# Optimization experiments

Measured on AMD Instinct MI355X. Metric: run time of the kernel, lower is better.

Reference implementation:

```python
import jax, jax.numpy as jnp
import numpy as np

N = 200000      # nodes
E_EDGES = 600000
G = 8000        # graphs
F_IN = 16
EMB = 128
L = 5           # GIN layers
C = 12          # targets
BN_EPS = 1e-5


def _bn(x, s, b, m, v):
    # BatchNorm1d in eval mode: normalize with stored running stats
    return (x - m) * jax.lax.rsqrt(v + BN_EPS) * s + b


def _mlp(x, w1, b1, s1, bb1, m1, v1, w2, b2, s2, bb2, m2, v2):
    h = jax.nn.relu(_bn(x @ w1 + b1, s1, bb1, m1, v1))
    return jax.nn.relu(_bn(h @ w2 + b2, s2, bb2, m2, v2))


def setup_inputs() -> dict:
    key = jax.random.key(0)
    ks = iter(jax.random.split(key, 64))
    inp = {}
    def nrm(shape, fan):
        return (jax.random.normal(next(ks), shape, jnp.float32) / np.sqrt(fan)).astype(jnp.float32)
    def bn_set(name, shape):
        inp[name + '_scale'] = jax.random.uniform(next(ks), shape, jnp.float32) * 0.5 + 0.75
        inp[name + '_bias'] = jax.random.normal(next(ks), shape, jnp.float32) * 0.1
        inp[name + '_mean'] = jax.random.normal(next(ks), shape, jnp.float32) * 0.1
        inp[name + '_var'] = jax.random.uniform(next(ks), shape, jnp.float32) * 0.5 + 0.75

    inp['x'] = jax.random.normal(next(ks), (N, F_IN), jnp.float32)
    src = jax.random.randint(next(ks), (E_EDGES,), 0, N, jnp.int32)
    dst = jax.random.randint(next(ks), (E_EDGES,), 0, N, jnp.int32)
    inp['edge_index'] = jnp.stack([src, dst])
    # sorted batch ids; every graph gets at least one node (avoid empty segment_max)
    inp['batch'] = jnp.sort(jnp.concatenate([
        jnp.arange(G, dtype=jnp.int32),
        jax.random.randint(next(ks), (N - G,), 0, G, jnp.int32)]))

    inp['init_w1'] = nrm((F_IN, EMB), F_IN)
    inp['init_b1'] = jnp.zeros((EMB,), jnp.float32)
    bn_set('init_bn1', (EMB,))
    inp['init_w2'] = nrm((EMB, EMB), EMB)
    inp['init_b2'] = jnp.zeros((EMB,), jnp.float32)
    bn_set('init_bn2', (EMB,))
    inp['init_lin_w'] = nrm((EMB, C), EMB)
    inp['init_lin_b'] = jnp.zeros((C,), jnp.float32)
    inp['eps'] = jnp.zeros((L,), jnp.float32)  # train_eps init 0.0
    inp['lw1'] = nrm((L, EMB, EMB), EMB)
    inp['lb1'] = jnp.zeros((L, EMB), jnp.float32)
    bn_set('lbn1', (L, EMB))
    inp['lw2'] = nrm((L, EMB, EMB), EMB)
    inp['lb2'] = jnp.zeros((L, EMB), jnp.float32)
    bn_set('lbn2', (L, EMB))
    inp['llin_w'] = nrm((L, EMB, C), EMB)
    inp['llin_b'] = jnp.zeros((L, C), jnp.float32)
    return inp


def _forward(edge_index, batch, x, init_w1, init_b1, init_bn1_scale, init_bn1_bias,
             init_bn1_mean, init_bn1_var, init_w2, init_b2, init_bn2_scale,
             init_bn2_bias, init_bn2_mean, init_bn2_var, init_lin_w, init_lin_b,
             eps, lw1, lb1, lbn1_scale, lbn1_bias, lbn1_mean, lbn1_var,
             lw2, lb2, lbn2_scale, lbn2_bias, lbn2_mean, lbn2_var, llin_w, llin_b):
    src, dst = edge_index[0], edge_index[1]
    h = _mlp(x, init_w1, init_b1, init_bn1_scale, init_bn1_bias, init_bn1_mean,
             init_bn1_var, init_w2, init_b2, init_bn2_scale, init_bn2_bias,
             init_bn2_mean, init_bn2_var)  # [N, EMB]
    # initial readout: linear then global max pool over graphs
    out = jax.ops.segment_max(h @ init_lin_w + init_lin_b, batch, num_segments=G)  # [G, C]
    for l in range(L):
        # GINConv: h <- MLP((1+eps)*h + sum_{j in N(i)} h_j)
        agg = jax.ops.segment_sum(h[src], dst, num_segments=N)  # gather + scatter-add
        h = _mlp((1.0 + eps[l]) * h + agg,
                 lw1[l], lb1[l], lbn1_scale[l], lbn1_bias[l], lbn1_mean[l], lbn1_var[l],
                 lw2[l], lb2[l], lbn2_scale[l], lbn2_bias[l], lbn2_mean[l], lbn2_var[l])
        # per-layer readout: global max pool then linear
        out = out + jax.ops.segment_max(h, batch, num_segments=G) @ llin_w[l] + llin_b[l]
    return out


def reference(x, edge_index, batch, init_w1, init_b1, init_bn1_scale, init_bn1_bias,
              init_bn1_mean, init_bn1_var, init_w2, init_b2, init_bn2_scale,
              init_bn2_bias, init_bn2_mean, init_bn2_var, init_lin_w, init_lin_b,
              eps, lw1, lb1, lbn1_scale, lbn1_bias, lbn1_mean, lbn1_var,
              lw2, lb2, lbn2_scale, lbn2_bias, lbn2_mean, lbn2_var, llin_w, llin_b):
    return _forward(edge_index, batch, x, init_w1, init_b1, init_bn1_scale,
                    init_bn1_bias, init_bn1_mean, init_bn1_var, init_w2, init_b2,
                    init_bn2_scale, init_bn2_bias, init_bn2_mean, init_bn2_var,
                    init_lin_w, init_lin_b, eps, lw1, lb1, lbn1_scale, lbn1_bias,
                    lbn1_mean, lbn1_var, lw2, lb2, lbn2_scale, lbn2_bias,
                    lbn2_mean, lbn2_var, llin_w, llin_b)
```

## Files before the change

kernel.cpp:

```cpp
#include <hip/hip_runtime.h>
#include <hip/hip_bf16.h>
#include <math.h>

#define EMB 128
#define CDIM 12
#define FIN 16
#define NLAYER 5
#define BN_EPS 1e-5f

typedef __attribute__((ext_vector_type(8))) _Float16 f16x8;
typedef __attribute__((ext_vector_type(2))) __fp16 fp16v2;
typedef __attribute__((ext_vector_type(4))) float f32x4;
typedef unsigned short ushort_t;

union h2u { fp16v2 h; unsigned u; };
union hu  { _Float16 h; ushort_t u; };

__device__ __forceinline__ void fsplit2(float a, float b, unsigned& hi, unsigned& lo) {
    h2u H; H.h = __builtin_amdgcn_cvt_pkrtz(a, b);
    float r0 = a - (float)H.h.x;
    float r1 = b - (float)H.h.y;
    h2u L; L.h = __builtin_amdgcn_cvt_pkrtz(r0, r1);
    hi = H.u; lo = L.u;
}

__device__ __forceinline__ unsigned pkrn(float x, float y) {
    hu A; A.h = (_Float16)x;
    hu B; B.h = (_Float16)y;
    return (unsigned)A.u | ((unsigned)B.u << 16);
}

__device__ __forceinline__ void acc8(float* f, uint4 v) {
    h2u c0, c1, c2, c3;
    c0.u = v.x; c1.u = v.y; c2.u = v.z; c3.u = v.w;
    f[0] += (float)c0.h.x; f[1] += (float)c0.h.y;
    f[2] += (float)c1.h.x; f[3] += (float)c1.h.y;
    f[4] += (float)c2.h.x; f[5] += (float)c2.h.y;
    f[6] += (float)c3.h.x; f[7] += (float)c3.h.y;
}

__device__ __forceinline__ unsigned swz(int node, unsigned byteoff) {
    return (unsigned)(node * 256 + byteoff) ^ (((unsigned)node & 7u) << 4);
}


__global__ __launch_bounds__(256) void k_gstart(const int* __restrict__ batch,
                                                int* __restrict__ gs, int N, int G) {
    int i = blockIdx.x * 256 + threadIdx.x;
    if (i >= N) return;
    if (i == 0) gs[0] = 0;
    else { int b = batch[i]; if (b != batch[i - 1]) gs[b] = i; }
    if (i == N - 1) gs[G] = N;
}

__global__ __launch_bounds__(256) void k_zero_i32(int* __restrict__ p, int n) {
    int i = blockIdx.x * 256 + threadIdx.x;
    if (i < n) p[i] = 0;
}

__global__ __launch_bounds__(256) void k_fill_i32(int* __restrict__ p, int val, int n) {
    int i = blockIdx.x * 256 + threadIdx.x;
    if (i < n) p[i] = val;
}

__global__ __launch_bounds__(256) void k_zero_f32(float* __restrict__ p, int n) {
    int i = blockIdx.x * 256 + threadIdx.x;
    if (i < n) p[i] = 0.f;
}

__global__ __launch_bounds__(128) void k_zero_dummy(ushort_t* __restrict__ a,
                                                    ushort_t* __restrict__ b, int N) {
    int i = threadIdx.x;
    a[(size_t)N * EMB + i] = 0;
    b[(size_t)N * EMB + i] = 0;
}

__global__ __launch_bounds__(256) void k_hist(const int* __restrict__ dst, int* __restrict__ cnt, int E) {
    int e = blockIdx.x * 256 + threadIdx.x;
    if (e < E) atomicAdd(&cnt[dst[e]], 1);
}

__global__ __launch_bounds__(256) void k_scan1(const int* __restrict__ cnt, int* __restrict__ rs,
                                               int* __restrict__ partials, int N) {
    __shared__ int tsum[256];
    int t = threadIdx.x;
    int base = blockIdx.x * 1024 + t * 4;
    int c[4];
    #pragma unroll
    for (int j = 0; j < 4; j++) c[j] = (base + j < N) ? ((cnt[base + j] + 3) & ~3) : 0;
    int s = c[0] + c[1] + c[2] + c[3];
    tsum[t] = s;
    __syncthreads();
    for (int off = 1; off < 256; off <<= 1) {
        int v = (t >= off) ? tsum[t - off] : 0;
        __syncthreads();
        tsum[t] += v;
        __syncthreads();
    }
    int run = tsum[t] - s;
    if (t == 255) partials[blockIdx.x] = tsum[255];
    #pragma unroll
    for (int j = 0; j < 4; j++) {
        if (base + j <= N) rs[base + j] = run;
        run += c[j];
    }
}

__global__ __launch_bounds__(256) void k_scan2(int* __restrict__ partials, int NB) {
    __shared__ int tmp[256];
    int t = threadIdx.x;
    int v = (t < NB) ? partials[t] : 0;
    tmp[t] = v;
    __syncthreads();
    for (int off = 1; off < 256; off <<= 1) {
        int u = (t >= off) ? tmp[t - off] : 0;
        __syncthreads();
        tmp[t] += u;
        __syncthreads();
    }
    if (t < NB) partials[t] = tmp[t] - v;
}

__global__ __launch_bounds__(256) void k_scan3(int* __restrict__ rs, const int* __restrict__ partials,
                                               int* __restrict__ cur_off, int N) {
    int t = threadIdx.x;
    int base = blockIdx.x * 1024 + t * 4;
    int add = partials[blockIdx.x];
    #pragma unroll
    for (int j = 0; j < 4; j++) {
        int i = base + j;
        if (i <= N) {
            int v = rs[i] + add;
            rs[i] = v;
            if (i < N) cur_off[i] = v;
        }
    }
}

__global__ __launch_bounds__(256) void k_fillslots(const int* __restrict__ src, const int* __restrict__ dst,
                                                   int* __restrict__ cur_off, int* __restrict__ csr_src, int E) {
    int e = blockIdx.x * 256 + threadIdx.x;
    if (e >= E) return;
    int d = dst[e];
    int pos = atomicAdd(&cur_off[d], 1);
    csr_src[pos] = src[e];
}


__global__ __launch_bounds__(256) void k_prep(
        const float* __restrict__ init_w1, const float* __restrict__ init_b1,
        const float* __restrict__ b1s, const float* __restrict__ b1b,
        const float* __restrict__ b1m, const float* __restrict__ b1v,
        const float* __restrict__ init_w2, const float* __restrict__ init_b2,
        const float* __restrict__ i_s, const float* __restrict__ i_b,
        const float* __restrict__ i_m, const float* __restrict__ i_v,
        const float* __restrict__ lw1, const float* __restrict__ lb1,
        const float* __restrict__ l1s, const float* __restrict__ l1b,
        const float* __restrict__ l1m, const float* __restrict__ l1v,
        const float* __restrict__ lw2, const float* __restrict__ lb2,
        const float* __restrict__ l2s, const float* __restrict__ l2b,
        const float* __restrict__ l2m, const float* __restrict__ l2v,
        const float* __restrict__ ilin_w, const float* __restrict__ ilin_b,
        ushort_t* __restrict__ WT, float* __restrict__ biasf,
        float* __restrict__ W1f, float* __restrict__ bias1f,
        ushort_t* __restrict__ WzT, float* __restrict__ biasz) {
    int j = blockIdx.x;
    int t = threadIdx.x;
    __shared__ float alpha[EMB];

    if (j == 12) {
        if (t < 16) biasz[t] = (t < CDIM) ? ilin_b[t] : 0.f;
        for (int i = t; i < 16 * EMB; i += 256) {
            int f = i >> 7, k = i & 127;
            float w = (f < CDIM) ? ilin_w[k * CDIM + f] : 0.f;
            hu x; x.h = (_Float16)w;
            WzT[i] = x.u;
        }
        return;
    }
    if (j == 11) {
        if (t < EMB) {
            float a = b1s[t] * rsqrtf(b1v[t] + BN_EPS);
            alpha[t] = a;
            bias1f[t] = init_b1[t] * a + (b1b[t] - b1m[t] * a);
        }
        __syncthreads();
        for (int i = t; i < FIN * EMB; i += 256) W1f[i] = init_w1[i] * alpha[i & 127];
        return;
    }

    const float *W, *lb, *s, *bb, *m, *v;
    if (j == 0)      { W = init_w2;            lb = init_b2;        s = i_s;           bb = i_b;           m = i_m;           v = i_v; }
    else if (j <= 5) { int l = j - 1; W = lw1 + l * 16384; lb = lb1 + l * 128; s = l1s + l * 128; bb = l1b + l * 128; m = l1m + l * 128; v = l1v + l * 128; }
    else             { int l = j - 6; W = lw2 + l * 16384; lb = lb2 + l * 128; s = l2s + l * 128; bb = l2b + l * 128; m = l2m + l * 128; v = l2v + l * 128; }
    if (t < EMB) {
        float a = s[t] * rsqrtf(v[t] + BN_EPS);
        alpha[t] = a;
        biasf[j * EMB + t] = lb[t] * a + (bb[t] - m[t] * a);
    }
    __syncthreads();
    for (int i = t; i < EMB * EMB; i += 256) {
        int k = i >> 7, f = i & 127;
        float w = W[i] * alpha[f];
        hu x; x.h = (_Float16)w;
        WT[j * 16384 + f * 128 + k] = x.u;
    }
}


template<int MODE>
__global__ __launch_bounds__(512, 4) void k_layer(
        const float* __restrict__ xin, const ushort_t* __restrict__ hin,
        ushort_t* __restrict__ hout, float* __restrict__ z,
        const ushort_t* __restrict__ W1T, const float* __restrict__ b1,
        const ushort_t* __restrict__ W2T, const float* __restrict__ b2,
        const ushort_t* __restrict__ WzT, const float* __restrict__ bz,
        const float* __restrict__ W1f, const float* __restrict__ b1f,
        const int* __restrict__ rs, const int* __restrict__ csr, const float* __restrict__ epsp,
        const int* __restrict__ batch, float* __restrict__ smax,
        int ntiles, int N) {
    constexpr int NT = (MODE == 1) ? 32 : 16;
    __shared__ ushort_t Ah[NT * 128], Al[NT * 128], Bh_[NT * 128], Bl_[NT * 128];
    __shared__ float W1s[(MODE == 0) ? FIN * EMB : 1];

    const int t = threadIdx.x;
    const int w = t >> 6;
    const int lane = t & 63;
    const int col = lane & 15, kg = lane >> 4;

    if (MODE == 0) {
        for (int i = t; i < FIN * EMB; i += 512) W1s[i] = W1f[i];
        __syncthreads();
    }

    f16x8 w1f[4], w2f[4], wzf[4];
    #pragma unroll
    for (int s = 0; s < 4; s++) {
        int off = (w * 16 + col) * EMB + s * 32 + kg * 8;
        w1f[s] = *(const f16x8*)(W1T + off);
        if (MODE == 1) w2f[s] = *(const f16x8*)(W2T + off);
        if (MODE == 0) {
            int zoff = col * EMB + s * 32 + kg * 8;
            wzf[s] = *(const f16x8*)(WzT + zoff);
        }
    }
    float4 bv1 = *(const float4*)&b1[w * 16 + kg * 4];
    float4 bv2, bvz;
    if (MODE == 1) bv2 = *(const float4*)&b2[w * 16 + kg * 4];
    if (MODE == 0) bvz = *(const float4*)&bz[kg * 4];
    float se = (MODE == 1) ? (1.f + epsp[0]) : 0.f;

    for (int tile = blockIdx.x; tile < ntiles; tile += gridDim.x) {
        const int n0 = tile * NT;

        if (MODE == 1) {
            const int nl = t >> 4, q2 = t & 15;
            const int nc = min(n0 + nl, N - 1);
            const uint4* hp = (const uint4*)hin;
            uint4 sv = hp[(size_t)nc * 16 + q2];
            float a[8] = {0.f, 0.f, 0.f, 0.f, 0.f, 0.f, 0.f, 0.f};
            acc8(a, sv);
            #pragma unroll
            for (int i = 0; i < 8; i++) a[i] *= se;
            int p = rs[nc], pe = rs[nc + 1];
            for (; p < pe; p += 4) {
                uint4 idx = *(const uint4*)&csr[p];
                uint4 v0 = hp[(size_t)idx.x * 16 + q2];
                uint4 v1 = hp[(size_t)idx.y * 16 + q2];
                uint4 v2 = hp[(size_t)idx.z * 16 + q2];
                uint4 v3 = hp[(size_t)idx.w * 16 + q2];
                acc8(a, v0); acc8(a, v1); acc8(a, v2); acc8(a, v3);
            }
            uint4 H, L;
            fsplit2(a[0], a[1], H.x, L.x);
            fsplit2(a[2], a[3], H.y, L.y);
            fsplit2(a[4], a[5], H.z, L.z);
            fsplit2(a[6], a[7], H.w, L.w);
            unsigned ad = swz(nl, (unsigned)q2 * 16);
            *(uint4*)((char*)Ah + ad) = H;
            *(uint4*)((char*)Al + ad) = L;
        } else {
            const int nl = t >> 5, q = t & 31;
            const int nc = min(n0 + nl, N - 1);
            float4 ba = *(const float4*)&b1f[q * 4];
            float a0 = ba.x, a1 = ba.y, a2 = ba.z, a3 = ba.w;
            const float* xp = xin + (size_t)nc * FIN;
            #pragma unroll
            for (int k = 0; k < FIN; k++) {
                float xk = xp[k];
                float4 wv = *(const float4*)&W1s[k * EMB + q * 4];
                a0 += xk * wv.x; a1 += xk * wv.y; a2 += xk * wv.z; a3 += xk * wv.w;
            }
            a0 = fmaxf(a0, 0.f); a1 = fmaxf(a1, 0.f); a2 = fmaxf(a2, 0.f); a3 = fmaxf(a3, 0.f);
            uint2 H, L;
            fsplit2(a0, a1, H.x, L.x);
            fsplit2(a2, a3, H.y, L.y);
            unsigned ad = swz(nl, (unsigned)q * 8);
            *(uint2*)((char*)Ah + ad) = H;
            *(uint2*)((char*)Al + ad) = L;
        }
        __syncthreads();

        {
            f32x4 aA0 = (f32x4){0.f, 0.f, 0.f, 0.f}, aB0 = aA0, aA1 = aA0, aB1 = aA0;
            #pragma unroll
            for (int s = 0; s < 4; s++) {
                unsigned bo = (unsigned)((s * 32 + kg * 8) * 2);
                f16x8 xh0 = *(const f16x8*)((const char*)Ah + swz(col, bo));
                f16x8 xl0 = *(const f16x8*)((const char*)Al + swz(col, bo));
                aA0 = __builtin_amdgcn_mfma_f32_16x16x32_f16(w1f[s], xh0, aA0, 0, 0, 0);
                aB0 = __builtin_amdgcn_mfma_f32_16x16x32_f16(w1f[s], xl0, aB0, 0, 0, 0);
                if (MODE == 1) {
                    f16x8 xh1 = *(const f16x8*)((const char*)Ah + swz(col + 16, bo));
                    f16x8 xl1 = *(const f16x8*)((const char*)Al + swz(col + 16, bo));
                    aA1 = __builtin_amdgcn_mfma_f32_16x16x32_f16(w1f[s], xh1, aA1, 0, 0, 0);
                    aB1 = __builtin_amdgcn_mfma_f32_16x16x32_f16(w1f[s], xl1, aB1, 0, 0, 0);
                }
            }
            #pragma unroll
            for (int sub = 0; sub < ((MODE == 1) ? 2 : 1); sub++) {
                f32x4 aa = sub ? aA1 : aA0, ab = sub ? aB1 : aB0;
                float y0 = fmaxf(aa[0] + ab[0] + bv1.x, 0.f);
                float y1 = fmaxf(aa[1] + ab[1] + bv1.y, 0.f);
                float y2 = fmaxf(aa[2] + ab[2] + bv1.z, 0.f);
                float y3 = fmaxf(aa[3] + ab[3] + bv1.w, 0.f);
                if (MODE == 0) {
                    int onode = n0 + col;
                    if (onode < N) {
                        uint2 P; P.x = pkrn(y0, y1); P.y = pkrn(y2, y3);
                        *(uint2*)&hout[(size_t)onode * EMB + w * 16 + kg * 4] = P;
                    }
                }
                uint2 H, L;
                fsplit2(y0, y1, H.x, L.x);
                fsplit2(y2, y3, H.y, L.y);
                unsigned ad = swz(col + sub * 16, (unsigned)(w * 32 + kg * 8));
                *(uint2*)((char*)Bh_ + ad) = H;
                *(uint2*)((char*)Bl_ + ad) = L;
            }
        }
        __syncthreads();

        if (MODE == 1) {
            f32x4 aA0 = (f32x4){0.f, 0.f, 0.f, 0.f}, aB0 = aA0, aA1 = aA0, aB1 = aA0;
            #pragma unroll
            for (int s = 0; s < 4; s++) {
                unsigned bo = (unsigned)((s * 32 + kg * 8) * 2);
                f16x8 xh0 = *(const f16x8*)((const char*)Bh_ + swz(col, bo));
                f16x8 xl0 = *(const f16x8*)((const char*)Bl_ + swz(col, bo));
                f16x8 xh1 = *(const f16x8*)((const char*)Bh_ + swz(col + 16, bo));
                f16x8 xl1 = *(const f16x8*)((const char*)Bl_ + swz(col + 16, bo));
                aA0 = __builtin_amdgcn_mfma_f32_16x16x32_f16(w2f[s], xh0, aA0, 0, 0, 0);
                aB0 = __builtin_amdgcn_mfma_f32_16x16x32_f16(w2f[s], xl0, aB0, 0, 0, 0);
                aA1 = __builtin_amdgcn_mfma_f32_16x16x32_f16(w2f[s], xh1, aA1, 0, 0, 0);
                aB1 = __builtin_amdgcn_mfma_f32_16x16x32_f16(w2f[s], xl1, aB1, 0, 0, 0);
            }
            #pragma unroll
            for (int sub = 0; sub < 2; sub++) {
                f32x4 aa = sub ? aA1 : aA0, ab = sub ? aB1 : aB0;
                int onode = n0 + col + sub * 16;
                float o0 = fmaxf(aa[0] + ab[0] + bv2.x, 0.f);
                float o1 = fmaxf(aa[1] + ab[1] + bv2.y, 0.f);
                float o2 = fmaxf(aa[2] + ab[2] + bv2.z, 0.f);
                float o3 = fmaxf(aa[3] + ab[3] + bv2.w, 0.f);
                if (hout && onode < N) {
                    uint2 P; P.x = pkrn(o0, o1); P.y = pkrn(o2, o3);
                    *(uint2*)&hout[(size_t)onode * EMB + w * 16 + kg * 4] = P;
                }
                bool valid = onode < N;
                float v0 = valid ? o0 : 0.f, v1 = valid ? o1 : 0.f;
                float v2 = valid ? o2 : 0.f, v3 = valid ? o3 : 0.f;
                int g = batch[min(onode, N - 1)];
                #pragma unroll
                for (int off = 1; off < 16; off <<= 1) {
                    float u0 = __shfl_up(v0, off, 16);
                    float u1 = __shfl_up(v1, off, 16);
                    float u2 = __shfl_up(v2, off, 16);
                    float u3 = __shfl_up(v3, off, 16);
                    int gg = __shfl_up(g, off, 16);
                    bool take = (col >= off) && (gg == g);
                    if (take) {
                        v0 = fmaxf(v0, u0); v1 = fmaxf(v1, u1);
                        v2 = fmaxf(v2, u2); v3 = fmaxf(v3, u3);
                    }
                }
                int gn = __shfl_down(g, 1, 16);
                bool tail = (col == 15) || (gn != g);
                if (tail) {
                    unsigned* sp = (unsigned*)&smax[(size_t)g * EMB + w * 16 + kg * 4];
                    atomicMax(sp + 0, __float_as_uint(v0));
                    atomicMax(sp + 1, __float_as_uint(v1));
                    atomicMax(sp + 2, __float_as_uint(v2));
                    atomicMax(sp + 3, __float_as_uint(v3));
                }
            }
        } else if (w == 0) {
            f32x4 aA0 = (f32x4){0.f, 0.f, 0.f, 0.f}, aB0 = aA0;
            #pragma unroll
            for (int s = 0; s < 4; s++) {
                unsigned bo = (unsigned)((s * 32 + kg * 8) * 2);
                f16x8 xh = *(const f16x8*)((const char*)Bh_ + swz(col, bo));
                f16x8 xl = *(const f16x8*)((const char*)Bl_ + swz(col, bo));
                aA0 = __builtin_amdgcn_mfma_f32_16x16x32_f16(wzf[s], xh, aA0, 0, 0, 0);
                aB0 = __builtin_amdgcn_mfma_f32_16x16x32_f16(wzf[s], xl, aB0, 0, 0, 0);
            }
            int onode = n0 + col;
            if (onode < N && kg < 3) {
                float4 o;
                o.x = aA0[0] + aB0[0] + bvz.x;
                o.y = aA0[1] + aB0[1] + bvz.y;
                o.z = aA0[2] + aB0[2] + bvz.z;
                o.w = aA0[3] + aB0[3] + bvz.w;
                *(float4*)&z[(size_t)onode * CDIM + kg * 4] = o;
            }
        }
    }
}


__global__ __launch_bounds__(64) void k_zmax(const float* __restrict__ z, const int* __restrict__ gs,
        float* __restrict__ out, int G) {
    int g = blockIdx.x;
    int t = threadIdx.x;
    if (t >= CDIM) return;
    int s0 = gs[g], e0 = gs[g + 1];
    float m = -INFINITY;
    for (int n = s0; n < e0; n++) m = fmaxf(m, z[(size_t)n * CDIM + t]);
    out[g * CDIM + t] = m;
}

__global__ __launch_bounds__(128) void k_comb(const float* __restrict__ smax,
        const float* __restrict__ llin_w, const float* __restrict__ llin_b,
        float* __restrict__ out, int G) {
    int g = blockIdx.x;
    int t = threadIdx.x;
    __shared__ float mv[NLAYER][EMB];
    #pragma unroll
    for (int l = 0; l < NLAYER; l++)
        mv[l][t] = smax[((size_t)l * G + g) * EMB + t];
    __syncthreads();
    __shared__ float parts_[8][16];
    int c = t & 15, half = t >> 4;
    float acc = 0.f;
    if (c < CDIM) {
        #pragma unroll
        for (int l = 0; l < NLAYER; l++) {
            const float* Wl = llin_w + l * EMB * CDIM;
            #pragma unroll
            for (int kk = 0; kk < 16; kk++) {
                int k = half * 16 + kk;
                acc += mv[l][k] * Wl[k * CDIM + c];
            }
        }
    }
    parts_[half][c] = acc;
    __syncthreads();
    if (t < CDIM) {
        float s = 0.f;
        #pragma unroll
        for (int hh = 0; hh < 8; hh++) s += parts_[hh][t];
        #pragma unroll
        for (int l = 0; l < NLAYER; l++) s += llin_b[l * CDIM + t];
        out[g * CDIM + t] += s;
    }
}


extern "C" void kernel_launch(void* const* d_in, const int* in_sizes, int n_in,
                              void* d_out, int out_size, void* d_ws, size_t ws_size,
                              hipStream_t stream) {
    const float* x        = (const float*)d_in[0];
    const int*   ei       = (const int*)d_in[1];
    const int*   batch    = (const int*)d_in[2];
    const float* init_w1  = (const float*)d_in[3];
    const float* init_b1  = (const float*)d_in[4];
    const float* ibn1_s   = (const float*)d_in[5];
    const float* ibn1_b   = (const float*)d_in[6];
    const float* ibn1_m   = (const float*)d_in[7];
    const float* ibn1_v   = (const float*)d_in[8];
    const float* init_w2  = (const float*)d_in[9];
    const float* init_b2  = (const float*)d_in[10];
    const float* ibn2_s   = (const float*)d_in[11];
    const float* ibn2_b   = (const float*)d_in[12];
    const float* ibn2_m   = (const float*)d_in[13];
    const float* ibn2_v   = (const float*)d_in[14];
    const float* ilin_w   = (const float*)d_in[15];
    const float* ilin_b   = (const float*)d_in[16];
    const float* eps      = (const float*)d_in[17];
    const float* lw1      = (const float*)d_in[18];
    const float* lb1      = (const float*)d_in[19];
    const float* lbn1_s   = (const float*)d_in[20];
    const float* lbn1_b   = (const float*)d_in[21];
    const float* lbn1_m   = (const float*)d_in[22];
    const float* lbn1_v   = (const float*)d_in[23];
    const float* lw2      = (const float*)d_in[24];
    const float* lb2      = (const float*)d_in[25];
    const float* lbn2_s   = (const float*)d_in[26];
    const float* lbn2_b   = (const float*)d_in[27];
    const float* lbn2_m   = (const float*)d_in[28];
    const float* lbn2_v   = (const float*)d_in[29];
    const float* llin_w   = (const float*)d_in[30];
    const float* llin_b   = (const float*)d_in[31];

    const int N = in_sizes[0] / FIN;
    const int E = in_sizes[1] / 2;
    const int G = out_size / CDIM;
    const int* src = ei;
    const int* dst = ei + E;
    float* out = (float*)d_out;

    const int EPADMAX = E + 3 * N;

    char* wp = (char*)d_ws;
    auto alloc = [&](size_t bytes) { char* p = wp; wp += (bytes + 255) & ~(size_t)255; return p; };
    ushort_t* WT    = (ushort_t*)alloc((size_t)11 * 16384 * 2);
    float*    biasf = (float*)alloc(11 * EMB * 4);
    float*    W1f   = (float*)alloc(FIN * EMB * 4);
    float*    bias1f= (float*)alloc(EMB * 4);
    ushort_t* WzT   = (ushort_t*)alloc(16 * EMB * 2);
    float*    biasz = (float*)alloc(16 * 4);
    int*      gs    = (int*)alloc((size_t)(G + 1) * 4);
    int*      rs    = (int*)alloc((size_t)(N + 1) * 4);
    int*      curoff= (int*)alloc((size_t)N * 4);
    int*      csr   = (int*)alloc((size_t)EPADMAX * 4);
    int*      parts = (int*)alloc(256 * 4);
    float*    zbuf  = (float*)alloc((size_t)N * CDIM * 4);
    float*    smax  = (float*)alloc((size_t)NLAYER * G * EMB * 4);
    ushort_t* bufP  = (ushort_t*)alloc((size_t)(N + 1) * EMB * 2);
    ushort_t* bufQ  = (ushort_t*)alloc((size_t)(N + 1) * EMB * 2);
    int*      cnt   = csr;

    const int NB = (N + 1 + 1023) / 1024;
    const int ntiles16 = (N + 15) / 16;
    const int ntiles32 = (N + 31) / 32;
    const int GRID = 2084;

    k_zero_f32<<<((NLAYER * G * EMB) + 255) / 256, 256, 0, stream>>>(smax, NLAYER * G * EMB);
    k_zero_dummy<<<1, 128, 0, stream>>>(bufP, bufQ, N);

    k_zero_i32<<<(N + 255) / 256, 256, 0, stream>>>(cnt, N);
    k_hist<<<(E + 255) / 256, 256, 0, stream>>>(dst, cnt, E);
    k_scan1<<<NB, 256, 0, stream>>>(cnt, rs, parts, N);
    k_scan2<<<1, 256, 0, stream>>>(parts, NB);
    k_scan3<<<NB, 256, 0, stream>>>(rs, parts, curoff, N);
    k_fill_i32<<<(EPADMAX + 255) / 256, 256, 0, stream>>>(csr, N, EPADMAX);
    k_fillslots<<<(E + 255) / 256, 256, 0, stream>>>(src, dst, curoff, csr, E);
    k_gstart<<<(N + 255) / 256, 256, 0, stream>>>(batch, gs, N, G);
    k_prep<<<13, 256, 0, stream>>>(init_w1, init_b1, ibn1_s, ibn1_b, ibn1_m, ibn1_v,
                                   init_w2, init_b2, ibn2_s, ibn2_b, ibn2_m, ibn2_v,
                                   lw1, lb1, lbn1_s, lbn1_b, lbn1_m, lbn1_v,
                                   lw2, lb2, lbn2_s, lbn2_b, lbn2_m, lbn2_v,
                                   ilin_w, ilin_b,
                                   WT, biasf, W1f, bias1f, WzT, biasz);

    k_layer<0><<<GRID, 512, 0, stream>>>(x, nullptr, bufQ, zbuf,
                                         WT, biasf,
                                         nullptr, nullptr,
                                         WzT, biasz,
                                         W1f, bias1f,
                                         nullptr, nullptr, nullptr,
                                         nullptr, nullptr, ntiles16, N);
    k_zmax<<<G, 64, 0, stream>>>(zbuf, gs, out, G);

    ushort_t* cur = bufQ;
    ushort_t* oth = bufP;
    for (int l = 0; l < NLAYER; l++) {
        ushort_t* houtl = (l == NLAYER - 1) ? nullptr : oth;
        k_layer<1><<<GRID, 512, 0, stream>>>(nullptr, cur, houtl, nullptr,
                                             WT + (size_t)(1 + l) * 16384, biasf + (1 + l) * EMB,
                                             WT + (size_t)(6 + l) * 16384, biasf + (6 + l) * EMB,
                                             nullptr, nullptr,
                                             nullptr, nullptr,
                                             rs, csr, eps + l,
                                             batch, smax + (size_t)l * G * EMB, ntiles32, N);
        ushort_t* tmp = cur; cur = oth; oth = tmp;
    }
    k_comb<<<G, 128, 0, stream>>>(smax, llin_w, llin_b, out, G);
}
```

Measured before the change: 711.9 us.

## Enlarge GIN layer tile to 64 nodes and issue neighbor gathers early

Raises the node tile in the message-passing layer kernel from 32 to 64, so each thread aggregates two nodes. The first group of four neighbor rows for both nodes is loaded before any accumulation, giving more gathers in flight per thread. The MFMA stages loop over four 16-node subtiles that share the register-held weights, and the grid becomes about two tiles per block. This doubles LDS use per block and adds register pressure under the 512x4 launch bounds, which may reduce occupancy.

```diff
diff --git a/kernel.cpp b/kernel.cpp
--- a/kernel.cpp
+++ b/kernel.cpp
@@ -219,7 +219,8 @@
         const int* __restrict__ rs, const int* __restrict__ csr, const float* __restrict__ epsp,
         const int* __restrict__ batch, float* __restrict__ smax,
         int ntiles, int N) {
-    constexpr int NT = (MODE == 1) ? 32 : 16;
+    constexpr int NT = (MODE == 1) ? 64 : 16;
+    constexpr int NSUB = (MODE == 1) ? 4 : 1;
     __shared__ ushort_t Ah[NT * 128], Al[NT * 128], Bh_[NT * 128], Bl_[NT * 128];
     __shared__ float W1s[(MODE == 0) ? FIN * EMB : 1];
 
@@ -250,33 +251,55 @@
     if (MODE == 0) bvz = *(const float4*)&bz[kg * 4];
     float se = (MODE == 1) ? (1.f + epsp[0]) : 0.f;
 
+    const int nlp = t >> 4, q2p = t & 15;
+
     for (int tile = blockIdx.x; tile < ntiles; tile += gridDim.x) {
         const int n0 = tile * NT;
 
         if (MODE == 1) {
-            const int nl = t >> 4, q2 = t & 15;
-            const int nc = min(n0 + nl, N - 1);
             const uint4* hp = (const uint4*)hin;
-            uint4 sv = hp[(size_t)nc * 16 + q2];
-            float a[8] = {0.f, 0.f, 0.f, 0.f, 0.f, 0.f, 0.f, 0.f};
-            acc8(a, sv);
-            #pragma unroll
-            for (int i = 0; i < 8; i++) a[i] *= se;
-            int p = rs[nc], pe = rs[nc + 1];
-            for (; p < pe; p += 4) {
+            const int ncA = min(n0 + nlp, N - 1);
+            const int ncB = min(n0 + nlp + 32, N - 1);
+            uint4 svA = hp[(size_t)ncA * 16 + q2p];
+            uint4 svB = hp[(size_t)ncB * 16 + q2p];
+            int pA = rs[ncA], peA = rs[ncA + 1];
+            int pB = rs[ncB], peB = rs[ncB + 1];
+            uint4 iA, iB;
+            if (pA < peA) iA = *(const uint4*)&csr[pA];
+            else { iA.x = iA.y = iA.z = iA.w = (unsigned)N; }
+            if (pB < peB) iB = *(const uint4*)&csr[pB];
+            else { iB.x = iB.y = iB.z = iB.w = (unsigned)N; }
+            uint4 rA0 = hp[(size_t)iA.x * 16 + q2p], rA1 = hp[(size_t)iA.y * 16 + q2p];
+            uint4 rA2 = hp[(size_t)iA.z * 16 + q2p], rA3 = hp[(size_t)iA.w * 16 + q2p];
+            uint4 rB0 = hp[(size_t)iB.x * 16 + q2p], rB1 = hp[(size_t)iB.y * 16 + q2p];
+            uint4 rB2 = hp[(size_t)iB.z * 16 + q2p], rB3 = hp[(size_t)iB.w * 16 + q2p];
+
+            float a[8] = {0.f,0.f,0.f,0.f,0.f,0.f,0.f,0.f};
+            float b[8] = {0.f,0.f,0.f,0.f,0.f,0.f,0.f,0.f};
+            acc8(a, svA); acc8(b, svB);
+            #pragma unroll
+            for (int i = 0; i < 8; i++) { a[i] *= se; b[i] *= se; }
+            acc8(a, rA0); acc8(a, rA1); acc8(a, rA2); acc8(a, rA3);
+            acc8(b, rB0); acc8(b, rB1); acc8(b, rB2); acc8(b, rB3);
+            for (int p = pA + 4; p < peA; p += 4) {
                 uint4 idx = *(const uint4*)&csr[p];
-                uint4 v0 = hp[(size_t)idx.x * 16 + q2];
-                uint4 v1 = hp[(size_t)idx.y * 16 + q2];
-                uint4 v2 = hp[(size_t)idx.z * 16 + q2];
-                uint4 v3 = hp[(size_t)idx.w * 16 + q2];
-                acc8(a, v0); acc8(a, v1); acc8(a, v2); acc8(a, v3);
+                acc8(a, hp[(size_t)idx.x * 16 + q2p]); acc8(a, hp[(size_t)idx.y * 16 + q2p]);
+                acc8(a, hp[(size_t)idx.z * 16 + q2p]); acc8(a, hp[(size_t)idx.w * 16 + q2p]);
+            }
+            for (int p = pB + 4; p < peB; p += 4) {
+                uint4 idx = *(const uint4*)&csr[p];
+                acc8(b, hp[(size_t)idx.x * 16 + q2p]); acc8(b, hp[(size_t)idx.y * 16 + q2p]);
+                acc8(b, hp[(size_t)idx.z * 16 + q2p]); acc8(b, hp[(size_t)idx.w * 16 + q2p]);
             }
             uint4 H, L;
-            fsplit2(a[0], a[1], H.x, L.x);
-            fsplit2(a[2], a[3], H.y, L.y);
-            fsplit2(a[4], a[5], H.z, L.z);
-            fsplit2(a[6], a[7], H.w, L.w);
-            unsigned ad = swz(nl, (unsigned)q2 * 16);
+            fsplit2(a[0], a[1], H.x, L.x); fsplit2(a[2], a[3], H.y, L.y);
+            fsplit2(a[4], a[5], H.z, L.z); fsplit2(a[6], a[7], H.w, L.w);
+            unsigned ad = swz(nlp, (unsigned)q2p * 16);
+            *(uint4*)((char*)Ah + ad) = H;
+            *(uint4*)((char*)Al + ad) = L;
+            fsplit2(b[0], b[1], H.x, L.x); fsplit2(b[2], b[3], H.y, L.y);
+            fsplit2(b[4], b[5], H.z, L.z); fsplit2(b[6], b[7], H.w, L.w);
+            ad = swz(nlp + 32, (unsigned)q2p * 16);
             *(uint4*)((char*)Ah + ad) = H;
             *(uint4*)((char*)Al + ad) = L;
         } else {
@@ -302,28 +325,26 @@
         __syncthreads();
 
         {
-            f32x4 aA0 = (f32x4){0.f, 0.f, 0.f, 0.f}, aB0 = aA0, aA1 = aA0, aB1 = aA0;
+            f32x4 aA[NSUB], aB[NSUB];
+            #pragma unroll
+            for (int j = 0; j < NSUB; j++) { aA[j] = (f32x4){0.f,0.f,0.f,0.f}; aB[j] = aA[j]; }
             #pragma unroll
             for (int s = 0; s < 4; s++) {
                 unsigned bo = (unsigned)((s * 32 + kg * 8) * 2);
-                f16x8 xh0 = *(const f16x8*)((const char*)Ah + swz(col, bo));
-                f16x8 xl0 = *(const f16x8*)((const char*)Al + swz(col, bo));
-                aA0 = __builtin_amdgcn_mfma_f32_16x16x32_f16(w1f[s], xh0, aA0, 0, 0, 0);
-                aB0 = __builtin_amdgcn_mfma_f32_16x16x32_f16(w1f[s], xl0, aB0, 0, 0, 0);
-                if (MODE == 1) {
-                    f16x8 xh1 = *(const f16x8*)((const char*)Ah + swz(col + 16, bo));
-                    f16x8 xl1 = *(const f16x8*)((const char*)Al + swz(col + 16, bo));
-                    aA1 = __builtin_amdgcn_mfma_f32_16x16x32_f16(w1f[s], xh1, aA1, 0, 0, 0);
-                    aB1 = __builtin_amdgcn_mfma_f32_16x16x32_f16(w1f[s], xl1, aB1, 0, 0, 0);
+                #pragma unroll
+                for (int j = 0; j < NSUB; j++) {
+                    f16x8 xh = *(const f16x8*)((const char*)Ah + swz(col + j * 16, bo));
+                    f16x8 xl = *(const f16x8*)((const char*)Al + swz(col + j * 16, bo));
+                    aA[j] = __builtin_amdgcn_mfma_f32_16x16x32_f16(w1f[s], xh, aA[j], 0, 0, 0);
+                    aB[j] = __builtin_amdgcn_mfma_f32_16x16x32_f16(w1f[s], xl, aB[j], 0, 0, 0);
                 }
             }
             #pragma unroll
-            for (int sub = 0; sub < ((MODE == 1) ? 2 : 1); sub++) {
-                f32x4 aa = sub ? aA1 : aA0, ab = sub ? aB1 : aB0;
-                float y0 = fmaxf(aa[0] + ab[0] + bv1.x, 0.f);
-                float y1 = fmaxf(aa[1] + ab[1] + bv1.y, 0.f);
-                float y2 = fmaxf(aa[2] + ab[2] + bv1.z, 0.f);
-                float y3 = fmaxf(aa[3] + ab[3] + bv1.w, 0.f);
+            for (int j = 0; j < NSUB; j++) {
+                float y0 = fmaxf(aA[j][0] + aB[j][0] + bv1.x, 0.f);
+                float y1 = fmaxf(aA[j][1] + aB[j][1] + bv1.y, 0.f);
+                float y2 = fmaxf(aA[j][2] + aB[j][2] + bv1.z, 0.f);
+                float y3 = fmaxf(aA[j][3] + aB[j][3] + bv1.w, 0.f);
                 if (MODE == 0) {
                     int onode = n0 + col;
                     if (onode < N) {
@@ -334,7 +355,7 @@
                 uint2 H, L;
                 fsplit2(y0, y1, H.x, L.x);
                 fsplit2(y2, y3, H.y, L.y);
-                unsigned ad = swz(col + sub * 16, (unsigned)(w * 32 + kg * 8));
+                unsigned ad = swz(col + j * 16, (unsigned)(w * 32 + kg * 8));
                 *(uint2*)((char*)Bh_ + ad) = H;
                 *(uint2*)((char*)Bl_ + ad) = L;
             }
@@ -342,27 +363,27 @@
         __syncthreads();
 
         if (MODE == 1) {
-            f32x4 aA0 = (f32x4){0.f, 0.f, 0.f, 0.f}, aB0 = aA0, aA1 = aA0, aB1 = aA0;
+            f32x4 aA[NSUB], aB[NSUB];
+            #pragma unroll
+            for (int j = 0; j < NSUB; j++) { aA[j] = (f32x4){0.f,0.f,0.f,0.f}; aB[j] = aA[j]; }
             #pragma unroll
             for (int s = 0; s < 4; s++) {
                 unsigned bo = (unsigned)((s * 32 + kg * 8) * 2);
-                f16x8 xh0 = *(const f16x8*)((const char*)Bh_ + swz(col, bo));
-                f16x8 xl0 = *(const f16x8*)((const char*)Bl_ + swz(col, bo));
-                f16x8 xh1 = *(const f16x8*)((const char*)Bh_ + swz(col + 16, bo));
-                f16x8 xl1 = *(const f16x8*)((const char*)Bl_ + swz(col + 16, bo));
-                aA0 = __builtin_amdgcn_mfma_f32_16x16x32_f16(w2f[s], xh0, aA0, 0, 0, 0);
-                aB0 = __builtin_amdgcn_mfma_f32_16x16x32_f16(w2f[s], xl0, aB0, 0, 0, 0);
-                aA1 = __builtin_amdgcn_mfma_f32_16x16x32_f16(w2f[s], xh1, aA1, 0, 0, 0);
-                aB1 = __builtin_amdgcn_mfma_f32_16x16x32_f16(w2f[s], xl1, aB1, 0, 0, 0);
-            }
-            #pragma unroll
-            for (int sub = 0; sub < 2; sub++) {
-                f32x4 aa = sub ? aA1 : aA0, ab = sub ? aB1 : aB0;
-                int onode = n0 + col + sub * 16;
-                float o0 = fmaxf(aa[0] + ab[0] + bv2.x, 0.f);
-                float o1 = fmaxf(aa[1] + ab[1] + bv2.y, 0.f);
-                float o2 = fmaxf(aa[2] + ab[2] + bv2.z, 0.f);
-                float o3 = fmaxf(aa[3] + ab[3] + bv2.w, 0.f);
+                #pragma unroll
+                for (int j = 0; j < NSUB; j++) {
+                    f16x8 xh = *(const f16x8*)((const char*)Bh_ + swz(col + j * 16, bo));
+                    f16x8 xl = *(const f16x8*)((const char*)Bl_ + swz(col + j * 16, bo));
+                    aA[j] = __builtin_amdgcn_mfma_f32_16x16x32_f16(w2f[s], xh, aA[j], 0, 0, 0);
+                    aB[j] = __builtin_amdgcn_mfma_f32_16x16x32_f16(w2f[s], xl, aB[j], 0, 0, 0);
+                }
+            }
+            #pragma unroll
+            for (int j = 0; j < NSUB; j++) {
+                int onode = n0 + col + j * 16;
+                float o0 = fmaxf(aA[j][0] + aB[j][0] + bv2.x, 0.f);
+                float o1 = fmaxf(aA[j][1] + aB[j][1] + bv2.y, 0.f);
+                float o2 = fmaxf(aA[j][2] + aB[j][2] + bv2.z, 0.f);
+                float o3 = fmaxf(aA[j][3] + aB[j][3] + bv2.w, 0.f);
                 if (hout && onode < N) {
                     uint2 P; P.x = pkrn(o0, o1); P.y = pkrn(o2, o3);
                     *(uint2*)&hout[(size_t)onode * EMB + w * 16 + kg * 4] = P;
@@ -532,8 +553,9 @@
 
     const int NB = (N + 1 + 1023) / 1024;
     const int ntiles16 = (N + 15) / 16;
-    const int ntiles32 = (N + 31) / 32;
-    const int GRID = 2084;
+    const int ntiles64 = (N + 63) / 64;
+    const int GRID0 = 2084;
+    const int GRID1 = (ntiles64 + 1) / 2;
 
     k_zero_f32<<<((NLAYER * G * EMB) + 255) / 256, 256, 0, stream>>>(smax, NLAYER * G * EMB);
     k_zero_dummy<<<1, 128, 0, stream>>>(bufP, bufQ, N);
@@ -553,26 +575,26 @@
                                    ilin_w, ilin_b,
                                    WT, biasf, W1f, bias1f, WzT, biasz);
 
-    k_layer<0><<<GRID, 512, 0, stream>>>(x, nullptr, bufQ, zbuf,
-                                         WT, biasf,
-                                         nullptr, nullptr,
-                                         WzT, biasz,
-                                         W1f, bias1f,
-                                         nullptr, nullptr, nullptr,
-                                         nullptr, nullptr, ntiles16, N);
+    k_layer<0><<<GRID0, 512, 0, stream>>>(x, nullptr, bufQ, zbuf,
+                                          WT, biasf,
+                                          nullptr, nullptr,
+                                          WzT, biasz,
+                                          W1f, bias1f,
+                                          nullptr, nullptr, nullptr,
+                                          nullptr, nullptr, ntiles16, N);
     k_zmax<<<G, 64, 0, stream>>>(zbuf, gs, out, G);
 
     ushort_t* cur = bufQ;
     ushort_t* oth = bufP;
     for (int l = 0; l < NLAYER; l++) {
         ushort_t* houtl = (l == NLAYER - 1) ? nullptr : oth;
-        k_layer<1><<<GRID, 512, 0, stream>>>(nullptr, cur, houtl, nullptr,
-                                             WT + (size_t)(1 + l) * 16384, biasf + (1 + l) * EMB,
-                                             WT + (size_t)(6 + l) * 16384, biasf + (6 + l) * EMB,
-                                             nullptr, nullptr,
-                                             nullptr, nullptr,
-                                             rs, csr, eps + l,
-                                             batch, smax + (size_t)l * G * EMB, ntiles32, N);
+        k_layer<1><<<GRID1, 512, 0, stream>>>(nullptr, cur, houtl, nullptr,
+                                              WT + (size_t)(1 + l) * 16384, biasf + (1 + l) * EMB,
+                                              WT + (size_t)(6 + l) * 16384, biasf + (6 + l) * EMB,
+                                              nullptr, nullptr,
+                                              nullptr, nullptr,
+                                              rs, csr, eps + l,
+                                              batch, smax + (size_t)l * G * EMB, ntiles64, N);
         ushort_t* tmp = cur; cur = oth; oth = tmp;
     }
     k_comb<<<G, 128, 0, stream>>>(smax, llin_w, llin_b, out, G);
```

Result: slower. 889.3 us (+24.9%).
